# Optimization experiments

Hardware: AMD Instinct MI355X
Metric: run time of the kernel (lower is better)

Reference implementation:

```python
import jax, jax.numpy as jnp
import numpy as np

N_NODES = 50000
N_EDGES = 1000000
D = 64
L = 3
BN_EPS = 1e-5


def setup_inputs() -> dict:
    key = jax.random.key(0)
    ks = jax.random.split(key, 6)
    x = jax.random.normal(ks[0], (N_NODES, D), dtype=jnp.float32)
    edge_src = jax.random.randint(ks[1], (N_EDGES,), 0, N_NODES)
    edge_dst = jax.random.randint(ks[2], (N_EDGES,), 0, N_NODES)
    edge_weight = jax.random.uniform(ks[3], (N_EDGES,), dtype=jnp.float32)
    W = jax.random.normal(ks[4], (L, D, D), dtype=jnp.float32) * (1.0 / np.sqrt(D))
    b = jnp.zeros((L, D), dtype=jnp.float32)
    prelu_a = jnp.full((L,), 0.25, dtype=jnp.float32)  # torch PReLU default init
    bn_gamma = jnp.ones((L, D), dtype=jnp.float32)
    bn_beta = jnp.zeros((L, D), dtype=jnp.float32)
    return {"x": x, "edge_src": edge_src, "edge_dst": edge_dst,
            "edge_weight": edge_weight, "W": W, "b": b, "prelu_a": prelu_a,
            "bn_gamma": bn_gamma, "bn_beta": bn_beta}


def reference(x, edge_src, edge_dst, edge_weight, W, b, prelu_a, bn_gamma, bn_beta):
    n = x.shape[0]
    h = x
    for i in range(L):
        h_in = h
        # GCNConv (normalize=False): aggregate edge_weight * (h @ W)[src] at dst, + bias
        xw = h @ W[i]                                       # [N, D]
        msg = edge_weight[:, None] * xw[edge_src]            # [E, D] gather
        agg = jax.ops.segment_sum(msg, edge_dst, num_segments=n) + b[i]
        # PReLU (single shared parameter per module)
        h = jnp.where(agg >= 0, agg, prelu_a[i] * agg)
        if i > 0:
            h = h + h_in
        # BatchNorm1d, training-mode batch statistics over nodes
        mean = jnp.mean(h, axis=0)
        var = jnp.mean((h - mean) ** 2, axis=0)  # biased variance, as torch BN
        h = bn_gamma[i] * (h - mean) * jax.lax.rsqrt(var + BN_EPS) + bn_beta[i]
        # dropout p=0.0 -> identity
    return h
```

## Files before the change

kernel.cpp:

```cpp
#include <hip/hip_runtime.h>
#include <hip/hip_fp16.h>

#define N_NODES 50000
#define N_EDGES 1000000
#define D 64
#define L 3
#define BN_EPS 1e-5f
#define NB_SCAN ((N_NODES + 255) / 256)
#define AGG_BLOCKS ((N_NODES + 31) / 32)
#define NXCD 8
#define BN_XSTRIDE (L * 2 * D)

__device__ inline int get_xcc() {
    int x;
    asm volatile("s_getreg_b32 %0, hwreg(HW_REG_XCC_ID)" : "=s"(x));
    return x & (NXCD - 1);
}

__device__ inline void bn_affine8(const float* __restrict__ bnsum_l,
                                  const float* __restrict__ gamma,
                                  const float* __restrict__ beta,
                                  int c, float& sc, float& sh) {
    float s1 = 0.f, s2 = 0.f;
#pragma unroll
    for (int x = 0; x < NXCD; x++) {
        s1 += bnsum_l[(size_t)x * BN_XSTRIDE + c];
        s2 += bnsum_l[(size_t)x * BN_XSTRIDE + D + c];
    }
    float mean = s1 * (1.f / N_NODES);
    float var = fmaf(-mean, mean, s2 * (1.f / N_NODES));
    float inv = rsqrtf(var + BN_EPS);
    sc = gamma[c] * inv;
    sh = fmaf(-mean, sc, beta[c]);
}

__device__ inline float unpack_w(unsigned int m) {
    __half_raw hr;
    hr.x = (unsigned short)(m & 0xffffu);
    __half h = *reinterpret_cast<__half*>(&hr);
    return __half2float(h);
}

__device__ inline float2 unpack_x2(unsigned int q) {
    __half2 h2 = *reinterpret_cast<__half2*>(&q);
    return __half22float2(h2);
}

__device__ inline float2 ntload_f2(const float2* p) {
    unsigned long long u = __builtin_nontemporal_load((const unsigned long long*)p);
    float2 r;
    r.x = __uint_as_float((unsigned int)(u & 0xffffffffull));
    r.y = __uint_as_float((unsigned int)(u >> 32));
    return r;
}

__device__ inline void ntstore_f2(float2* p, float2 v) {
    unsigned long long u =
        ((unsigned long long)__float_as_uint(v.y) << 32) | (unsigned long long)__float_as_uint(v.x);
    __builtin_nontemporal_store(u, (unsigned long long*)p);
}

__global__ void init_kernel(int* __restrict__ counts8, float* __restrict__ bnsum8) {
    int i = blockIdx.x * blockDim.x + threadIdx.x;
    int stride = gridDim.x * blockDim.x;
    for (int j = i; j < NXCD * N_NODES; j += stride) counts8[j] = 0;
    for (int j = i; j < NXCD * BN_XSTRIDE; j += stride) bnsum8[j] = 0.f;
}

__global__ void count_kernel(const int* __restrict__ dst, int* __restrict__ counts8,
                             unsigned short* __restrict__ rankx) {
    int xcd = get_xcc();
    int* mycnt = counts8 + (size_t)xcd * N_NODES;
    int i = blockIdx.x * blockDim.x + threadIdx.x;
    int stride = gridDim.x * blockDim.x;
    for (int e = i; e < N_EDGES; e += stride) {
        int r = atomicAdd(&mycnt[dst[e]], 1);
        rankx[e] = (unsigned short)(r | (xcd << 13));
    }
}

__global__ __launch_bounds__(256) void scanA_kernel(const int* __restrict__ counts8,
                                                    int* __restrict__ counts,
                                                    int* __restrict__ blocksum) {
    __shared__ int buf[256];
    int t = threadIdx.x, b = blockIdx.x;
    int i = b * 256 + t;
    int v = 0;
    if (i < N_NODES) {
#pragma unroll
        for (int x = 0; x < NXCD; x++) v += counts8[(size_t)x * N_NODES + i];
        counts[i] = v;
    }
    buf[t] = v;
    __syncthreads();
    for (int off = 128; off > 0; off >>= 1) {
        if (t < off) buf[t] += buf[t + off];
        __syncthreads();
    }
    if (t == 0) blocksum[b] = buf[0];
}

__global__ __launch_bounds__(256) void scanB_kernel(const int* __restrict__ blocksum,
                                                    int* __restrict__ blockoff,
                                                    int* __restrict__ row_ptr) {
    __shared__ int buf[256];
    int t = threadIdx.x;
    int v = (t < NB_SCAN) ? blocksum[t] : 0;
    buf[t] = v;
    __syncthreads();
    for (int off = 1; off < 256; off <<= 1) {
        int u = (t >= off) ? buf[t - off] : 0;
        __syncthreads();
        buf[t] += u;
        __syncthreads();
    }
    if (t < NB_SCAN) blockoff[t] = buf[t] - v;
    if (t == NB_SCAN - 1) row_ptr[N_NODES] = buf[t];
}

__global__ __launch_bounds__(256) void scanC_kernel(const int* __restrict__ counts,
                                                    const int* __restrict__ blockoff,
                                                    int* __restrict__ row_ptr) {
    __shared__ int buf[256];
    int t = threadIdx.x, b = blockIdx.x;
    int i = b * 256 + t;
    int v = (i < N_NODES) ? counts[i] : 0;
    buf[t] = v;
    __syncthreads();
    for (int off = 1; off < 256; off <<= 1) {
        int u = (t >= off) ? buf[t - off] : 0;
        __syncthreads();
        buf[t] += u;
        __syncthreads();
    }
    if (i < N_NODES) row_ptr[i] = blockoff[b] + buf[t] - v;
}

__global__ __launch_bounds__(256) void offs8_kernel(const int* __restrict__ counts8,
                                                    const int* __restrict__ row_ptr,
                                                    int* __restrict__ offs8) {
    int i = blockIdx.x * blockDim.x + threadIdx.x;
    if (i < N_NODES) {
        int base = row_ptr[i];
#pragma unroll
        for (int x = 0; x < NXCD; x++) {
            offs8[(size_t)x * N_NODES + i] = base;
            base += counts8[(size_t)x * N_NODES + i];
        }
    }
}

__global__ void fill_kernel(const int* __restrict__ src, const int* __restrict__ dst,
                            const float* __restrict__ w,
                            const unsigned short* __restrict__ rankx,
                            const int* __restrict__ offs8,
                            unsigned int* __restrict__ em) {
    int i = blockIdx.x * blockDim.x + threadIdx.x;
    int stride = gridDim.x * blockDim.x;
    for (int e = i; e < N_EDGES; e += stride) {
        int d = dst[e];
        unsigned rx = rankx[e];
        int p = offs8[(size_t)(rx >> 13) * N_NODES + d] + (int)(rx & 0x1fffu);
        __half h = __float2half_rn(w[e]);
        unsigned short wb = reinterpret_cast<__half_raw*>(&h)->x;
        em[p] = ((unsigned int)src[e] << 16) | (unsigned int)wb;
    }
}

__global__ __launch_bounds__(256) void gemm_kernel(const float* __restrict__ hraw,
                                                   const float* __restrict__ bnsum_p,
                                                   const float* __restrict__ gamma_p,
                                                   const float* __restrict__ beta_p,
                                                   const float* __restrict__ Wl,
                                                   __half* __restrict__ xw) {
    __shared__ float aff[2][D];
    int tid = threadIdx.x, lane = tid & 63, wave = tid >> 6;
    if (tid < D) {
        float sc = 1.f, sh = 0.f;
        if (bnsum_p) bn_affine8(bnsum_p, gamma_p, beta_p, tid, sc, sh);
        aff[0][tid] = sc;
        aff[1][tid] = sh;
    }
    __syncthreads();
    float Wreg[D];
    float biasc = 0.f;
#pragma unroll
    for (int k = 0; k < D; k++) {
        float wkc = Wl[k * D + lane];
        biasc = fmaf(aff[1][k], wkc, biasc);
        Wreg[k] = wkc * aff[0][k];
    }
    int gw = blockIdx.x * 4 + wave, nw = gridDim.x * 4;
    for (int v = gw; v < N_NODES; v += nw) {
        const float* hp = hraw + (size_t)__builtin_amdgcn_readfirstlane(v) * D;
        float acc = biasc;
#pragma unroll
        for (int k = 0; k < D; k++) acc = fmaf(hp[k], Wreg[k], acc);
        xw[v * D + lane] = __float2half_rn(acc);
    }
}

__global__ __launch_bounds__(256) void agg_kernel(const uint2* __restrict__ xw,
                                                  const int* __restrict__ row_ptr,
                                                  const unsigned int* __restrict__ em,
                                                  const float* __restrict__ bl,
                                                  const float* __restrict__ pa,
                                                  const float* __restrict__ hraw_prev,
                                                  const float* __restrict__ bnsum_p,
                                                  const float* __restrict__ gamma_p,
                                                  const float* __restrict__ beta_p,
                                                  float* __restrict__ hpre,
                                                  float* __restrict__ bnsum_l) {
    __shared__ float r1[D], r2[D];
    int tid = threadIdx.x, lane = tid & 63;
    int sub = tid >> 4;
    int fl = lane & 15;
    int srcbase = lane & 48;
    if (tid < D) { r1[tid] = 0.f; r2[tid] = 0.f; }
    __syncthreads();

    float al = pa[0];
    int c0 = 4 * fl;
    float4 bias = ((const float4*)bl)[fl];
    float sc0 = 0, sc1 = 0, sc2 = 0, sc3 = 0, sh0 = 0, sh1 = 0, sh2 = 0, sh3 = 0;
    if (hraw_prev) {
        bn_affine8(bnsum_p, gamma_p, beta_p, c0 + 0, sc0, sh0);
        bn_affine8(bnsum_p, gamma_p, beta_p, c0 + 1, sc1, sh1);
        bn_affine8(bnsum_p, gamma_p, beta_p, c0 + 2, sc2, sh2);
        bn_affine8(bnsum_p, gamma_p, beta_p, c0 + 3, sc3, sh3);
    }
    float t1_0 = 0, t1_1 = 0, t1_2 = 0, t1_3 = 0;
    float t2_0 = 0, t2_1 = 0, t2_2 = 0, t2_3 = 0;

    int base = blockIdx.x * 16 + sub;
#pragma unroll 1
    for (int n = 0; n < 2; n++) {
        int v = base * 2 + n;
        if (v >= N_NODES) break;
        int e0 = row_ptr[v], e1 = row_ptr[v + 1];
        float a0 = 0, a1 = 0, a2 = 0, a3 = 0, b0 = 0, b1 = 0, b2 = 0, b3 = 0;
        for (int e = e0; e < e1; e += 16) {
            unsigned mo = (e + fl < e1) ? __builtin_nontemporal_load(em + e + fl) : 0u;
            unsigned mj[16];
            uint2 q[16];
#pragma unroll
            for (int j = 0; j < 16; j++) {
                mj[j] = (unsigned)__shfl((int)mo, srcbase + j, 64);
                q[j] = xw[(mj[j] >> 16) * 16 + fl];
            }
#pragma unroll
            for (int j = 0; j < 16; j++) {
                float w = unpack_w(mj[j]);
                float2 f01 = unpack_x2(q[j].x);
                float2 f23 = unpack_x2(q[j].y);
                if (j & 1) {
                    b0 = fmaf(w, f01.x, b0); b1 = fmaf(w, f01.y, b1);
                    b2 = fmaf(w, f23.x, b2); b3 = fmaf(w, f23.y, b3);
                } else {
                    a0 = fmaf(w, f01.x, a0); a1 = fmaf(w, f01.y, a1);
                    a2 = fmaf(w, f23.x, a2); a3 = fmaf(w, f23.y, a3);
                }
            }
        }
        float h0 = a0 + b0 + bias.x;
        float h1 = a1 + b1 + bias.y;
        float h2 = a2 + b2 + bias.z;
        float h3 = a3 + b3 + bias.w;
        h0 = h0 >= 0.f ? h0 : al * h0;
        h1 = h1 >= 0.f ? h1 : al * h1;
        h2 = h2 >= 0.f ? h2 : al * h2;
        h3 = h3 >= 0.f ? h3 : al * h3;
        if (hraw_prev) {
            float2 p01 = ntload_f2((const float2*)hraw_prev + v * 32 + 2 * fl);
            float2 p23 = ntload_f2((const float2*)hraw_prev + v * 32 + 2 * fl + 1);
            h0 = fmaf(p01.x, sc0, h0 + sh0);
            h1 = fmaf(p01.y, sc1, h1 + sh1);
            h2 = fmaf(p23.x, sc2, h2 + sh2);
            h3 = fmaf(p23.y, sc3, h3 + sh3);
        }
        ntstore_f2((float2*)hpre + v * 32 + 2 * fl, make_float2(h0, h1));
        ntstore_f2((float2*)hpre + v * 32 + 2 * fl + 1, make_float2(h2, h3));
        t1_0 += h0; t1_1 += h1; t1_2 += h2; t1_3 += h3;
        t2_0 = fmaf(h0, h0, t2_0);
        t2_1 = fmaf(h1, h1, t2_1);
        t2_2 = fmaf(h2, h2, t2_2);
        t2_3 = fmaf(h3, h3, t2_3);
    }
    t1_0 += __shfl_xor(t1_0, 16, 64); t1_0 += __shfl_xor(t1_0, 32, 64);
    t1_1 += __shfl_xor(t1_1, 16, 64); t1_1 += __shfl_xor(t1_1, 32, 64);
    t1_2 += __shfl_xor(t1_2, 16, 64); t1_2 += __shfl_xor(t1_2, 32, 64);
    t1_3 += __shfl_xor(t1_3, 16, 64); t1_3 += __shfl_xor(t1_3, 32, 64);
    t2_0 += __shfl_xor(t2_0, 16, 64); t2_0 += __shfl_xor(t2_0, 32, 64);
    t2_1 += __shfl_xor(t2_1, 16, 64); t2_1 += __shfl_xor(t2_1, 32, 64);
    t2_2 += __shfl_xor(t2_2, 16, 64); t2_2 += __shfl_xor(t2_2, 32, 64);
    t2_3 += __shfl_xor(t2_3, 16, 64); t2_3 += __shfl_xor(t2_3, 32, 64);
    if (lane < 16) {
        atomicAdd(&r1[c0 + 0], t1_0);
        atomicAdd(&r1[c0 + 1], t1_1);
        atomicAdd(&r1[c0 + 2], t1_2);
        atomicAdd(&r1[c0 + 3], t1_3);
        atomicAdd(&r2[c0 + 0], t2_0);
        atomicAdd(&r2[c0 + 1], t2_1);
        atomicAdd(&r2[c0 + 2], t2_2);
        atomicAdd(&r2[c0 + 3], t2_3);
    }
    __syncthreads();
    if (tid < D) {
        float* myb = bnsum_l + (size_t)get_xcc() * BN_XSTRIDE;
        atomicAdd(&myb[tid], r1[tid]);
        atomicAdd(&myb[D + tid], r2[tid]);
    }
}

__global__ __launch_bounds__(256) void bnapply_kernel(const float* __restrict__ hpre,
                                                      const float* __restrict__ bnsum_p,
                                                      const float* __restrict__ gamma_p,
                                                      const float* __restrict__ beta_p,
                                                      float* __restrict__ out) {
    __shared__ float aff[2][D];
    int tid = threadIdx.x;
    if (tid < D) {
        float sc, sh;
        bn_affine8(bnsum_p, gamma_p, beta_p, tid, sc, sh);
        aff[0][tid] = sc;
        aff[1][tid] = sh;
    }
    __syncthreads();
    int i = blockIdx.x * blockDim.x + tid;
    int stride = gridDim.x * blockDim.x;
    const int NQ = N_NODES * D / 4;
    for (int j = i; j < NQ; j += stride) {
        float4 hv = ((const float4*)hpre)[j];
        int c = (j * 4) & 63;
        float4 o;
        o.x = fmaf(hv.x, aff[0][c + 0], aff[1][c + 0]);
        o.y = fmaf(hv.y, aff[0][c + 1], aff[1][c + 1]);
        o.z = fmaf(hv.z, aff[0][c + 2], aff[1][c + 2]);
        o.w = fmaf(hv.w, aff[0][c + 3], aff[1][c + 3]);
        ((float4*)out)[j] = o;
    }
}

extern "C" void kernel_launch(void* const* d_in, const int* in_sizes, int n_in,
                              void* d_out, int out_size, void* d_ws, size_t ws_size,
                              hipStream_t stream) {
    const float* x     = (const float*)d_in[0];
    const int*   esrc  = (const int*)d_in[1];
    const int*   edst  = (const int*)d_in[2];
    const float* ew    = (const float*)d_in[3];
    const float* W     = (const float*)d_in[4];
    const float* b     = (const float*)d_in[5];
    const float* pa    = (const float*)d_in[6];
    const float* gamma = (const float*)d_in[7];
    const float* beta  = (const float*)d_in[8];
    float* out = (float*)d_out;

    char* ws = (char*)d_ws;
    size_t off = 0;
    auto alloc = [&](size_t bytes) -> char* {
        char* p = ws + off;
        off = (off + bytes + 255) & ~(size_t)255;
        return p;
    };
    int*            counts8  = (int*)alloc((size_t)NXCD * N_NODES * 4);
    int*            counts   = (int*)alloc((size_t)N_NODES * 4);
    int*            row_ptr  = (int*)alloc((size_t)(N_NODES + 1) * 4);
    int*            offs8    = (int*)alloc((size_t)NXCD * N_NODES * 4);
    int*            blocksum = (int*)alloc((size_t)NB_SCAN * 4);
    int*            blockoff = (int*)alloc((size_t)NB_SCAN * 4);
    unsigned short* rankx    = (unsigned short*)alloc((size_t)N_EDGES * 2);
    unsigned int*   em       = (unsigned int*)alloc((size_t)N_EDGES * 4);
    __half*         xw       = (__half*)alloc((size_t)N_NODES * D * 2);
    float*          hpre1    = (float*)alloc((size_t)N_NODES * D * 4);
    float*          bnsum8   = (float*)alloc((size_t)NXCD * BN_XSTRIDE * 4);

    init_kernel<<<512, 256, 0, stream>>>(counts8, bnsum8);
    count_kernel<<<2048, 256, 0, stream>>>(edst, counts8, rankx);
    scanA_kernel<<<NB_SCAN, 256, 0, stream>>>(counts8, counts, blocksum);
    scanB_kernel<<<1, 256, 0, stream>>>(blocksum, blockoff, row_ptr);
    scanC_kernel<<<NB_SCAN, 256, 0, stream>>>(counts, blockoff, row_ptr);
    offs8_kernel<<<NB_SCAN, 256, 0, stream>>>(counts8, row_ptr, offs8);
    fill_kernel<<<2048, 256, 0, stream>>>(esrc, edst, ew, rankx, offs8, em);

    float* hbuf[L] = {out, hpre1, out};
    for (int i = 0; i < L; i++) {
        const float* hin = (i == 0) ? x : hbuf[i - 1];
        const float* bns = (i == 0) ? nullptr : bnsum8 + (i - 1) * 2 * D;
        const float* gmp = (i == 0) ? nullptr : gamma + (i - 1) * D;
        const float* btp = (i == 0) ? nullptr : beta + (i - 1) * D;
        gemm_kernel<<<512, 256, 0, stream>>>(hin, bns, gmp, btp, W + (size_t)i * D * D, xw);
        agg_kernel<<<AGG_BLOCKS, 256, 0, stream>>>((const uint2*)xw, row_ptr, em,
                                                   b + i * D, pa + i,
                                                   (i == 0) ? nullptr : hbuf[i - 1],
                                                   bns, gmp, btp,
                                                   hbuf[i], bnsum8 + i * 2 * D);
    }
    bnapply_kernel<<<2048, 256, 0, stream>>>(hbuf[2], bnsum8 + 2 * 2 * D,
                                             gamma + 2 * D, beta + 2 * D, out);
}
```

Measured before the change: 227.8 us.

## Merge two-node edge loop with prefetch, fuse offs8 into scan, enlarge gemm grid

The aggregation kernel now walks the contiguous edge range of two consecutive nodes as one loop. It splits each edge's contribution into A or B accumulators by comparing the edge index to the boundary, and prefetches the next 16 edge metadata words while the current batch is processed. The offs8 kernel is folded into scanC, so one launch and a row_ptr reread go away. The gemm grid is doubled. The predicated split doubles the FMA count per edge in exchange for fewer loop tails and better latency hiding.

```diff
diff --git a/kernel.cpp b/kernel.cpp
--- a/kernel.cpp
+++ b/kernel.cpp
@@ -119,8 +119,10 @@
 }
 
 __global__ __launch_bounds__(256) void scanC_kernel(const int* __restrict__ counts,
+                                                    const int* __restrict__ counts8,
                                                     const int* __restrict__ blockoff,
-                                                    int* __restrict__ row_ptr) {
+                                                    int* __restrict__ row_ptr,
+                                                    int* __restrict__ offs8) {
     __shared__ int buf[256];
     int t = threadIdx.x, b = blockIdx.x;
     int i = b * 256 + t;
@@ -133,15 +135,9 @@
         buf[t] += u;
         __syncthreads();
     }
-    if (i < N_NODES) row_ptr[i] = blockoff[b] + buf[t] - v;
-}
-
-__global__ __launch_bounds__(256) void offs8_kernel(const int* __restrict__ counts8,
-                                                    const int* __restrict__ row_ptr,
-                                                    int* __restrict__ offs8) {
-    int i = blockIdx.x * blockDim.x + threadIdx.x;
     if (i < N_NODES) {
-        int base = row_ptr[i];
+        int base = blockoff[b] + buf[t] - v;
+        row_ptr[i] = base;
 #pragma unroll
         for (int x = 0; x < NXCD; x++) {
             offs8[(size_t)x * N_NODES + i] = base;
@@ -232,15 +228,16 @@
     float t1_0 = 0, t1_1 = 0, t1_2 = 0, t1_3 = 0;
     float t2_0 = 0, t2_1 = 0, t2_2 = 0, t2_3 = 0;
 
-    int base = blockIdx.x * 16 + sub;
-#pragma unroll 1
-    for (int n = 0; n < 2; n++) {
-        int v = base * 2 + n;
-        if (v >= N_NODES) break;
-        int e0 = row_ptr[v], e1 = row_ptr[v + 1];
-        float a0 = 0, a1 = 0, a2 = 0, a3 = 0, b0 = 0, b1 = 0, b2 = 0, b3 = 0;
-        for (int e = e0; e < e1; e += 16) {
-            unsigned mo = (e + fl < e1) ? __builtin_nontemporal_load(em + e + fl) : 0u;
+    int v0 = (blockIdx.x * 16 + sub) * 2;
+    if (v0 < N_NODES) {
+        int2 e01 = *(const int2*)(row_ptr + v0);
+        int e0 = e01.x, m = e01.y;
+        int e2 = row_ptr[v0 + 2];
+        float A0 = 0, A1 = 0, A2 = 0, A3 = 0, B0 = 0, B1 = 0, B2 = 0, B3 = 0;
+        unsigned mo = (e0 + fl < e2) ? __builtin_nontemporal_load(em + e0 + fl) : 0u;
+        for (int e = e0; e < e2; e += 16) {
+            unsigned mo_nx =
+                (e + 16 + fl < e2) ? __builtin_nontemporal_load(em + e + 16 + fl) : 0u;
             unsigned mj[16];
             uint2 q[16];
 #pragma unroll
@@ -251,40 +248,45 @@
 #pragma unroll
             for (int j = 0; j < 16; j++) {
                 float w = unpack_w(mj[j]);
+                bool isB = (e + j) >= m;
+                float wa = isB ? 0.f : w;
+                float wb = isB ? w : 0.f;
                 float2 f01 = unpack_x2(q[j].x);
                 float2 f23 = unpack_x2(q[j].y);
-                if (j & 1) {
-                    b0 = fmaf(w, f01.x, b0); b1 = fmaf(w, f01.y, b1);
-                    b2 = fmaf(w, f23.x, b2); b3 = fmaf(w, f23.y, b3);
-                } else {
-                    a0 = fmaf(w, f01.x, a0); a1 = fmaf(w, f01.y, a1);
-                    a2 = fmaf(w, f23.x, a2); a3 = fmaf(w, f23.y, a3);
-                }
+                A0 = fmaf(wa, f01.x, A0); A1 = fmaf(wa, f01.y, A1);
+                A2 = fmaf(wa, f23.x, A2); A3 = fmaf(wa, f23.y, A3);
+                B0 = fmaf(wb, f01.x, B0); B1 = fmaf(wb, f01.y, B1);
+                B2 = fmaf(wb, f23.x, B2); B3 = fmaf(wb, f23.y, B3);
             }
+            mo = mo_nx;
         }
-        float h0 = a0 + b0 + bias.x;
-        float h1 = a1 + b1 + bias.y;
-        float h2 = a2 + b2 + bias.z;
-        float h3 = a3 + b3 + bias.w;
-        h0 = h0 >= 0.f ? h0 : al * h0;
-        h1 = h1 >= 0.f ? h1 : al * h1;
-        h2 = h2 >= 0.f ? h2 : al * h2;
-        h3 = h3 >= 0.f ? h3 : al * h3;
-        if (hraw_prev) {
-            float2 p01 = ntload_f2((const float2*)hraw_prev + v * 32 + 2 * fl);
-            float2 p23 = ntload_f2((const float2*)hraw_prev + v * 32 + 2 * fl + 1);
-            h0 = fmaf(p01.x, sc0, h0 + sh0);
-            h1 = fmaf(p01.y, sc1, h1 + sh1);
-            h2 = fmaf(p23.x, sc2, h2 + sh2);
-            h3 = fmaf(p23.y, sc3, h3 + sh3);
+#pragma unroll
+        for (int n = 0; n < 2; n++) {
+            int v = v0 + n;
+            float h0 = (n ? B0 : A0) + bias.x;
+            float h1 = (n ? B1 : A1) + bias.y;
+            float h2 = (n ? B2 : A2) + bias.z;
+            float h3 = (n ? B3 : A3) + bias.w;
+            h0 = h0 >= 0.f ? h0 : al * h0;
+            h1 = h1 >= 0.f ? h1 : al * h1;
+            h2 = h2 >= 0.f ? h2 : al * h2;
+            h3 = h3 >= 0.f ? h3 : al * h3;
+            if (hraw_prev) {
+                float2 p01 = ntload_f2((const float2*)hraw_prev + v * 32 + 2 * fl);
+                float2 p23 = ntload_f2((const float2*)hraw_prev + v * 32 + 2 * fl + 1);
+                h0 = fmaf(p01.x, sc0, h0 + sh0);
+                h1 = fmaf(p01.y, sc1, h1 + sh1);
+                h2 = fmaf(p23.x, sc2, h2 + sh2);
+                h3 = fmaf(p23.y, sc3, h3 + sh3);
+            }
+            ntstore_f2((float2*)hpre + v * 32 + 2 * fl, make_float2(h0, h1));
+            ntstore_f2((float2*)hpre + v * 32 + 2 * fl + 1, make_float2(h2, h3));
+            t1_0 += h0; t1_1 += h1; t1_2 += h2; t1_3 += h3;
+            t2_0 = fmaf(h0, h0, t2_0);
+            t2_1 = fmaf(h1, h1, t2_1);
+            t2_2 = fmaf(h2, h2, t2_2);
+            t2_3 = fmaf(h3, h3, t2_3);
         }
-        ntstore_f2((float2*)hpre + v * 32 + 2 * fl, make_float2(h0, h1));
-        ntstore_f2((float2*)hpre + v * 32 + 2 * fl + 1, make_float2(h2, h3));
-        t1_0 += h0; t1_1 += h1; t1_2 += h2; t1_3 += h3;
-        t2_0 = fmaf(h0, h0, t2_0);
-        t2_1 = fmaf(h1, h1, t2_1);
-        t2_2 = fmaf(h2, h2, t2_2);
-        t2_3 = fmaf(h3, h3, t2_3);
     }
     t1_0 += __shfl_xor(t1_0, 16, 64); t1_0 += __shfl_xor(t1_0, 32, 64);
     t1_1 += __shfl_xor(t1_1, 16, 64); t1_1 += __shfl_xor(t1_1, 32, 64);
@@ -378,8 +380,7 @@
     count_kernel<<<2048, 256, 0, stream>>>(edst, counts8, rankx);
     scanA_kernel<<<NB_SCAN, 256, 0, stream>>>(counts8, counts, blocksum);
     scanB_kernel<<<1, 256, 0, stream>>>(blocksum, blockoff, row_ptr);
-    scanC_kernel<<<NB_SCAN, 256, 0, stream>>>(counts, blockoff, row_ptr);
-    offs8_kernel<<<NB_SCAN, 256, 0, stream>>>(counts8, row_ptr, offs8);
+    scanC_kernel<<<NB_SCAN, 256, 0, stream>>>(counts, counts8, blockoff, row_ptr, offs8);
     fill_kernel<<<2048, 256, 0, stream>>>(esrc, edst, ew, rankx, offs8, em);
 
     float* hbuf[L] = {out, hpre1, out};
@@ -388,7 +389,7 @@
         const float* bns = (i == 0) ? nullptr : bnsum8 + (i - 1) * 2 * D;
         const float* gmp = (i == 0) ? nullptr : gamma + (i - 1) * D;
         const float* btp = (i == 0) ? nullptr : beta + (i - 1) * D;
-        gemm_kernel<<<512, 256, 0, stream>>>(hin, bns, gmp, btp, W + (size_t)i * D * D, xw);
+        gemm_kernel<<<1024, 256, 0, stream>>>(hin, bns, gmp, btp, W + (size_t)i * D * D, xw);
         agg_kernel<<<AGG_BLOCKS, 256, 0, stream>>>((const uint2*)xw, row_ptr, em,
                                                    b + i * D, pa + i,
                                                    (i == 0) ? nullptr : hbuf[i - 1],
```

Result: no change. 227.6 us (-0.1%).
